# Kernel tuning notes

Hardware: AMD Instinct MI355X
Metric: run time of the kernel (lower is better)

The kernel has to match this reference:

```python
import jax, jax.numpy as jnp
import numpy as np

N_FLUID = 20000
N_BOX = 10000
PARTICLE_RADIUS = 0.025
FILTER_EXTENT = 1.5 * 6 * PARTICLE_RADIUS   # radius_scale * 6 * particle_radius = 0.225
RADIUS = 0.5 * FILTER_EXTENT                # neighbor search radius = 0.1125
DT = 1.0 / 50.0
KS = 4                                      # kernel size per axis
K3 = KS * KS * KS
LAYER_CH = [32, 64, 64, 3]
GRAVITY = jnp.array([0.0, -9.81, 0.0], jnp.float32)


def _radius_search(query, source, radius, exclude_self=False):
    """Brute-force (chunked) fixed radius search in numpy; returns (query_idx, src_idx)."""
    r2 = radius * radius
    s2 = (source ** 2).sum(1)
    qs, ss = [], []
    chunk = 2048
    for i0 in range(0, query.shape[0], chunk):
        q = query[i0:i0 + chunk]
        d2 = (q ** 2).sum(1)[:, None] + s2[None, :] - 2.0 * (q @ source.T)
        m = d2 < r2
        if exclude_self:  # radius_search_ignore_query_points=True
            rows = np.arange(q.shape[0])
            m[rows, i0 + rows] = False
        qq, sj = np.nonzero(m)
        qs.append((qq + i0).astype(np.int32))
        ss.append(sj.astype(np.int32))
    return np.concatenate(qs), np.concatenate(ss)


def _glorot(rng, shape):
    std = np.sqrt(2.0 / (shape[-2] + shape[-1]))
    return (rng.randn(*shape) * std).astype(np.float32)


def setup_inputs() -> dict:
    rng = np.random.RandomState(0)
    side = (N_FLUID / 8000.0) ** (1.0 / 3.0)  # rest density (2*particle_radius)^-3 = 8000/m^3
    pos = (rng.rand(N_FLUID, 3) * side).astype(np.float32)
    vel = (rng.randn(N_FLUID, 3) * 0.5).astype(np.float32)
    box = (rng.rand(N_BOX, 3) * side).astype(np.float32)
    bn = rng.randn(N_BOX, 3)
    box_feats = (bn / np.linalg.norm(bn, axis=1, keepdims=True)).astype(np.float32)
    # Neighbor search runs on gravity-integrated positions, exactly as in forward.
    g = np.array([0.0, -9.81, 0.0], np.float32)
    vel2 = vel + DT * g
    pos2 = pos + DT * (vel2 + vel) * 0.5
    ff_q, ff_s = _radius_search(pos2, pos2, RADIUS, exclude_self=True)
    fo_q, fo_s = _radius_search(pos2, box, RADIUS)
    inp = dict(pos=pos, vel=vel, box=box, box_feats=box_feats,
               ff_q=ff_q, ff_s=ff_s, fo_q=fo_q, fo_s=fo_s)
    inp['w_cf0'] = _glorot(rng, (KS, KS, KS, 4, LAYER_CH[0]))
    inp['w_co0'] = _glorot(rng, (KS, KS, KS, 3, LAYER_CH[0]))
    inp['w_d0'] = _glorot(rng, (4, LAYER_CH[0]))
    inp['b_d0'] = np.zeros(LAYER_CH[0], np.float32)
    in_chs = [3 * LAYER_CH[0], LAYER_CH[1], LAYER_CH[2]]
    for i in range(1, 4):
        ci, co = in_chs[i - 1], LAYER_CH[i]
        inp['w_c%d' % i] = _glorot(rng, (KS, KS, KS, ci, co))
        inp['w_d%d' % i] = _glorot(rng, (ci, co))
        inp['b_d%d' % i] = np.zeros(co, np.float32)
    return {k: jnp.asarray(v) for k, v in inp.items()}


def ball_to_cube(u):
    """Volume-preserving unit-ball -> unit-cube map (sphere->cylinder->cube). u: [E,3]."""
    x, y, z = u[:, 0], u[:, 1], u[:, 2]
    eps = 1e-12
    sq = x * x + y * y + z * z
    norm = jnp.sqrt(sq + eps)
    # sphere -> cylinder
    cap = 1.25 * z * z > x * x + y * y
    s_cap = jnp.sqrt(3.0 * norm / (norm + jnp.abs(z) + eps))
    s_side = norm / jnp.sqrt(x * x + y * y + eps)
    s = jnp.where(cap, s_cap, s_side)
    xc, yc = x * s, y * s
    zc = jnp.where(cap, jnp.sign(z) * norm, 1.5 * z)
    nz = sq > eps
    xc = jnp.where(nz, xc, 0.0)
    yc = jnp.where(nz, yc, 0.0)
    zc = jnp.where(nz, zc, 0.0)
    # cylinder -> cube: area-preserving (concentric) disc -> square on xy
    rxy = jnp.sqrt(xc * xc + yc * yc + eps)
    xbig = jnp.abs(yc) <= jnp.abs(xc)
    dx = jnp.where(jnp.abs(xc) > eps, xc, 1.0)
    dy = jnp.where(jnp.abs(yc) > eps, yc, 1.0)
    c4pi = 4.0 / jnp.pi
    tx = jnp.sign(xc) * rxy
    ty = jnp.sign(yc) * rxy
    xq = jnp.where(xbig, tx, ty * c4pi * jnp.arctan(xc / dy))
    yq = jnp.where(xbig, tx * c4pi * jnp.arctan(yc / dx), ty)
    nxy = xc * xc + yc * yc > eps
    xq = jnp.where(nxy, xq, 0.0)
    yq = jnp.where(nxy, yq, 0.0)
    return jnp.stack([xq, yq, zc], axis=-1)


def cconv(Wk, feat_src, q_idx, s_idx, pos_s, pos_q, nq):
    """ContinuousConv: window * trilinear kernel interp * gather, scatter-reduce to queries.
    Wk: [KS,KS,KS,Cin,Cout]. Returns [nq,Cout]."""
    d = (pos_s[s_idx] - pos_q[q_idx]) * (1.0 / RADIUS)    # [E,3] in unit ball
    r2 = jnp.sum(d * d, axis=-1)
    win = jnp.clip((1.0 - r2) ** 3, 0.0, 1.0)             # poly6 window
    g = (ball_to_cube(d) + 1.0) * (0.5 * (KS - 1))        # align_corners grid coords [0,KS-1]
    g0f = jnp.floor(g)
    f = g - g0f
    g0 = g0f.astype(jnp.int32)
    s = feat_src[s_idx] * win[:, None]                    # [E,Cin]
    cin = feat_src.shape[1]
    # accumulate per (query, kernel-cell) then one dense GEMM with the kernel
    G = jnp.zeros((nq * K3, cin), feat_src.dtype)
    for c in range(8):
        b = jnp.array([(c >> 2) & 1, (c >> 1) & 1, c & 1], jnp.int32)
        idx = jnp.clip(g0 + b[None, :], 0, KS - 1)        # [E,3]
        w = jnp.prod(jnp.where(b[None, :] == 1, f, 1.0 - f), axis=-1)  # trilinear wt [E]
        cell = (idx[:, 0] * KS + idx[:, 1]) * KS + idx[:, 2]
        G = G.at[q_idx * K3 + cell].add(w[:, None] * s)
    return jnp.einsum('nkc,kco->no', G.reshape(nq, K3, cin), Wk.reshape(K3, cin, -1))


def reference(pos, vel, box, box_feats, ff_q, ff_s, fo_q, fo_s,
              w_cf0, w_co0, w_d0, b_d0,
              w_c1, w_d1, b_d1, w_c2, w_d2, b_d2, w_c3, w_d3, b_d3):
    n = pos.shape[0]
    vel2 = vel + DT * GRAVITY
    pos2 = pos + DT * (vel2 + vel) * 0.5
    fl = jnp.concatenate([jnp.ones_like(pos[:, :1]), vel2], axis=-1)  # [N,4]
    a_cf = cconv(w_cf0, fl, ff_q, ff_s, pos2, pos2, n)
    a_co = cconv(w_co0, box_feats, fo_q, fo_s, box, pos2, n)
    a_df = fl @ w_d0 + b_d0
    x = jnp.concatenate([a_co, a_cf, a_df], axis=-1)  # [N,96]
    for wc, wd, bd in ((w_c1, w_d1, b_d1), (w_c2, w_d2, b_d2), (w_c3, w_d3, b_d3)):
        h = jax.nn.relu(x)
        y = cconv(wc, h, ff_q, ff_s, pos2, pos2, n) + h @ wd + bd
        x = y + x if y.shape[-1] == x.shape[-1] else y
    pos_correction = x * (1.0 / 128.0)
    pos_new = pos2 + pos_correction
    vel_new = (pos_new - pos) * (1.0 / DT)
    return pos_new, vel_new
```

## Files before the change

kernel.cpp:

```cpp
#include <hip/hip_runtime.h>
#include <algorithm>

#define DT_F 0.02f
#define INV_R (1.0f / 0.1125f)

typedef __attribute__((ext_vector_type(8))) short short8;
typedef __attribute__((ext_vector_type(4))) float float4v;

static inline int cdiv(int a, int b) { return (a + b - 1) / b; }

__device__ __forceinline__ float sgnf(float v) {
    return (v > 0.f) ? 1.f : ((v < 0.f) ? -1.f : 0.f);
}

__device__ __forceinline__ unsigned short f2bf(float f) {
    union { float f; unsigned u; } v; v.f = f;
    return (unsigned short)((v.u + 0x7fffu + ((v.u >> 16) & 1u)) >> 16);
}
__device__ __forceinline__ float bf2f(unsigned short h) {
    union { unsigned u; float f; } v; v.u = ((unsigned)h) << 16;
    return v.f;
}

__device__ __forceinline__ void ball_to_cube_dev(float x, float y, float z,
                                                 float& ox, float& oy, float& oz) {
    const float eps = 1e-12f;
    float sq = x * x + y * y + z * z;
    float nrm = sqrtf(sq + eps);
    float xy2 = x * x + y * y;
    bool cap = 1.25f * z * z > xy2;
    float s_cap = sqrtf(3.f * nrm / (nrm + fabsf(z) + eps));
    float s_side = nrm / sqrtf(xy2 + eps);
    float s = cap ? s_cap : s_side;
    float xc = x * s, yc = y * s;
    float zc = cap ? sgnf(z) * nrm : 1.5f * z;
    if (!(sq > eps)) { xc = 0.f; yc = 0.f; zc = 0.f; }
    float rxy = sqrtf(xc * xc + yc * yc + eps);
    bool xbig = fabsf(yc) <= fabsf(xc);
    float dx = (fabsf(xc) > eps) ? xc : 1.f;
    float dy = (fabsf(yc) > eps) ? yc : 1.f;
    const float c4pi = 1.27323954473516276f;
    float tx = sgnf(xc) * rxy, ty = sgnf(yc) * rxy;
    float xq = xbig ? tx : ty * c4pi * atanf(xc / dy);
    float yq = xbig ? tx * c4pi * atanf(yc / dx) : ty;
    if (!(xc * xc + yc * yc > eps)) { xq = 0.f; yq = 0.f; }
    ox = xq; oy = yq; oz = zc;
}

__global__ void prep_kernel(const float* __restrict__ pos, const float* __restrict__ vel,
                            int n, float* __restrict__ pos2, float* __restrict__ fl) {
    int i = blockIdx.x * blockDim.x + threadIdx.x;
    if (i >= n) return;
    float v0 = vel[i * 3 + 0], v1 = vel[i * 3 + 1], v2 = vel[i * 3 + 2];
    float u0 = v0, u1 = v1 + DT_F * (-9.81f), u2 = v2;
    pos2[i * 3 + 0] = pos[i * 3 + 0] + DT_F * (u0 + v0) * 0.5f;
    pos2[i * 3 + 1] = pos[i * 3 + 1] + DT_F * (u1 + v1) * 0.5f;
    pos2[i * 3 + 2] = pos[i * 3 + 2] + DT_F * (u2 + v2) * 0.5f;
    fl[i * 4 + 0] = 1.f;
    fl[i * 4 + 1] = u0;
    fl[i * 4 + 2] = u1;
    fl[i * 4 + 3] = u2;
}

__global__ void row_ptr_kernel(const int* __restrict__ q_idx, int E, int nq,
                               int* __restrict__ row_ptr) {
    int q = blockIdx.x * blockDim.x + threadIdx.x;
    if (q > nq) return;
    int lo = 0, hi = E;
    while (lo < hi) {
        int mid = (lo + hi) >> 1;
        if (q_idx[mid] < q) lo = mid + 1; else hi = mid;
    }
    row_ptr[q] = lo;
}

__global__ void edge_geom_kernel(const float* __restrict__ posq, const float* __restrict__ poss,
                                 const int* __restrict__ q_idx, const int* __restrict__ s_idx,
                                 int E, float* __restrict__ wgt, uint2* __restrict__ cells,
                                 uint4* __restrict__ edata) {
    int e = blockIdx.x * blockDim.x + threadIdx.x;
    if (e >= E) return;
    int q = q_idx[e], s = s_idx[e];
    float dx = (poss[s * 3 + 0] - posq[q * 3 + 0]) * INV_R;
    float dy = (poss[s * 3 + 1] - posq[q * 3 + 1]) * INV_R;
    float dz = (poss[s * 3 + 2] - posq[q * 3 + 2]) * INV_R;
    float r2 = dx * dx + dy * dy + dz * dz;
    float w1 = 1.f - r2;
    float win = fminf(fmaxf(w1 * w1 * w1, 0.f), 1.f);
    float bx, by, bz;
    ball_to_cube_dev(dx, dy, dz, bx, by, bz);
    float gx = (bx + 1.f) * 1.5f, gy = (by + 1.f) * 1.5f, gz = (bz + 1.f) * 1.5f;
    int ix = min(max((int)floorf(gx), 0), 2);
    int iy = min(max((int)floorf(gy), 0), 2);
    int iz = min(max((int)floorf(gz), 0), 2);
    float fx = gx - (float)ix, fy = gy - (float)iy, fz = gz - (float)iz;
    float wv[8];
    unsigned int cl[8];
#pragma unroll
    for (int c = 0; c < 8; c++) {
        int cbx = (c >> 2) & 1, cby = (c >> 1) & 1, cbz = c & 1;
        int jx = ix + cbx, jy = iy + cby, jz = iz + cbz;
        cl[c] = (unsigned int)((jx * 4 + jy) * 4 + jz);
        wv[c] = win * (cbx ? fx : 1.f - fx) * (cby ? fy : 1.f - fy) * (cbz ? fz : 1.f - fz);
    }
    float4* wp = (float4*)(wgt + (size_t)e * 8);
    wp[0] = make_float4(wv[0], wv[1], wv[2], wv[3]);
    wp[1] = make_float4(wv[4], wv[5], wv[6], wv[7]);
    uint2 cp;
    cp.x = cl[0] | (cl[1] << 8) | (cl[2] << 16) | (cl[3] << 24);
    cp.y = cl[4] | (cl[5] << 8) | (cl[6] << 16) | (cl[7] << 24);
    cells[e] = cp;
#pragma unroll
    for (int w = 0; w < 4; w++) {
        int pa = w >> 1, pb = w & 1;
        int cby = pa ^ (iy & 1), cbz = pb ^ (iz & 1);
        int cA = cby * 2 + cbz;
        uint4 d;
        d.x = __float_as_uint(wv[cA]);
        d.y = __float_as_uint(wv[cA + 4]);
        d.z = cl[cA] | (cl[cA + 4] << 8);
        d.w = (unsigned)s;
        edata[(size_t)w * E + e] = d;
    }
}

__global__ void dense0_kernel(const float* __restrict__ fl, const float* __restrict__ w,
                              const float* __restrict__ b, int n, float* __restrict__ x96) {
    int i = blockIdx.x * blockDim.x + threadIdx.x;
    if (i >= n * 32) return;
    int q = i >> 5, o = i & 31;
    float acc = b[o];
#pragma unroll
    for (int c = 0; c < 4; c++) acc += fl[q * 4 + c] * w[c * 32 + o];
    x96[(size_t)q * 96 + 64 + o] = acc;
}

__global__ void init_out_kernel(float* __restrict__ C, const float* __restrict__ bias,
                                const float* __restrict__ resid, int n, int co, int ldc) {
    int i = blockIdx.x * blockDim.x + threadIdx.x;
    if (i >= n * co) return;
    int q = i / co, o = i - q * co;
    float v = bias ? bias[o] : 0.f;
    if (resid) v += resid[(size_t)q * ldc + o];
    C[(size_t)q * ldc + o] = v;
}

__global__ void wt_kernel(const float* __restrict__ wc, const float* __restrict__ wd,
                          int ci, int co, int K, unsigned short* __restrict__ Wt) {
    int i = blockIdx.x * blockDim.x + threadIdx.x;
    if (i >= co * K) return;
    int n = i / K, k = i - n * K;
    float v = (k < 64 * ci) ? wc[(size_t)k * co + n] : wd[(size_t)(k - 64 * ci) * co + n];
    Wt[i] = f2bf(v);
}

__global__ void wt3_kernel(const float* __restrict__ wc, unsigned short* __restrict__ Wt) {
    int i = blockIdx.x * blockDim.x + threadIdx.x;
    if (i >= 192 * 64) return;
    int j = i >> 6, k = i & 63;
    int cell = j / 3, o = j - cell * 3;
    Wt[i] = f2bf(wc[((size_t)cell * 64 + k) * 3 + o]);
}

__global__ void relu_bf16_kernel(const float* __restrict__ x, int n,
                                 unsigned short* __restrict__ h) {
    int i = blockIdx.x * blockDim.x + threadIdx.x;
    if (i < n) h[i] = f2bf(fmaxf(x[i], 0.f));
}

template <int CIN>
__global__ __launch_bounds__(256) void build_G0_par(
    const float* __restrict__ feat, const uint4* __restrict__ edata, int E,
    const int* __restrict__ row_ptr, int q0, float* __restrict__ G) {
    __shared__ float Gs[4 * 64 * 8];
    int lq = blockIdx.x, q = q0 + lq, t = threadIdx.x;
    int wave = t >> 6, lane = t & 63;
    int j = lane >> 4, k = (lane >> 3) & 1, ch = lane & 7;
    for (int i = t; i < 2048; i += 256) Gs[i] = 0.f;
    __syncthreads();
    int e0 = row_ptr[q], e1 = row_ptr[q + 1];
    int cnt = e1 - e0;
    if (cnt > 0) {
        int last = e1 - 1;
        const uint4* ed = edata + (size_t)wave * E;
        int nIt = (cnt + 3) >> 2;
        uint4 dA = ed[min(e0 + j, last)];
        uint4 dB = ed[min(e0 + 4 + j, last)];
        float fA = (ch < CIN) ? feat[(size_t)dA.w * CIN + ch] : 0.f;
        float* Gr = Gs + j * 512;
        for (int i = 0; i < nIt; i++) {
            uint4 dC = ed[min(e0 + (i + 2) * 4 + j, last)];
            float fB = (ch < CIN) ? feat[(size_t)dB.w * CIN + ch] : 0.f;
            bool v = (e0 + i * 4 + j) < e1;
            float w = v ? (k ? __uint_as_float(dA.y) : __uint_as_float(dA.x)) : 0.f;
            int cell = (int)((dA.z >> (k * 8)) & 255u);
            Gr[cell * 8 + ch] += w * fA;
            dA = dB; dB = dC; fA = fB;
        }
    }
    __syncthreads();
    size_t base = (size_t)lq * 64 * CIN;
    for (int i = t; i < 64 * CIN; i += 256) {
        int cell = i / CIN, c = i - cell * CIN;
        int o = cell * 8 + c;
        G[base + i] = Gs[o] + Gs[512 + o] + Gs[1024 + o] + Gs[1536 + o];
    }
}

template <int CIN>
__global__ __launch_bounds__(256) void build_G_mfma(
    const unsigned short* __restrict__ hb,
    const float* __restrict__ wgt, const uint2* __restrict__ cells,
    const int* __restrict__ s_idx, const int* __restrict__ row_ptr,
    int q0, unsigned short* __restrict__ G) {
    constexpr int LDK = 72;
    constexpr int CP = CIN / 2;
    constexpr int NT = CIN / 16;
    __shared__ unsigned short S[64 * LDK];
    __shared__ unsigned short Ft[CIN * LDK];
    int lq = blockIdx.x, q = q0 + lq, t = threadIdx.x;
    int wave = t >> 6, lane = t & 63;
    int e0 = row_ptr[q], e1 = row_ptr[q + 1];
    int nE = e1 - e0;
    float4v acc[NT];
#pragma unroll
    for (int i = 0; i < NT; i++) acc[i] = (float4v){0.f, 0.f, 0.f, 0.f};

    for (int c0 = 0; c0 < nE; c0 += 64) {
        int cnt = min(64, nE - c0);
        __syncthreads();
        for (int i = t; i < 64 * LDK / 2; i += 256) ((unsigned int*)S)[i] = 0u;
        for (int i = t; i < 64 * CP; i += 256) {
            int e = i / CP, cp = i - e * CP;
            unsigned v = 0u;
            if (e < cnt) {
                int s = s_idx[e0 + c0 + e];
                v = ((const unsigned int*)hb)[(size_t)s * CP + cp];
            }
            Ft[(2 * cp) * LDK + e] = (unsigned short)(v & 0xffffu);
            Ft[(2 * cp + 1) * LDK + e] = (unsigned short)(v >> 16);
        }
        {
            int e = t >> 2, cpair = t & 3;
            if (e < cnt) {
                int ee = e0 + c0 + e;
                uint2 cp = cells[ee];
                float w0 = wgt[(size_t)ee * 8 + cpair * 2];
                float w1 = wgt[(size_t)ee * 8 + cpair * 2 + 1];
                unsigned word = (cpair < 2) ? cp.x : cp.y;
                int sh = (cpair & 1) * 16;
                int cell0 = (int)((word >> sh) & 255u);
                int cell1 = (int)((word >> (sh + 8)) & 255u);
                S[cell0 * LDK + e] = f2bf(w0);
                S[cell1 * LDK + e] = f2bf(w1);
            }
        }
        __syncthreads();
        int kq = lane >> 4, mrow = lane & 15;
#pragma unroll
        for (int ks = 0; ks < 2; ks++) {
            int kk = ks * 32 + kq * 8;
            short8 a = *(const short8*)(S + (wave * 16 + mrow) * LDK + kk);
#pragma unroll
            for (int nt = 0; nt < NT; nt++) {
                short8 b = *(const short8*)(Ft + (nt * 16 + mrow) * LDK + kk);
                acc[nt] = __builtin_amdgcn_mfma_f32_16x16x32_bf16(a, b, acc[nt], 0, 0, 0);
            }
        }
    }
    unsigned short* Go = G + (size_t)lq * (size_t)(65 * CIN);
    int col = lane & 15, rq = lane >> 4;
#pragma unroll
    for (int nt = 0; nt < NT; nt++) {
#pragma unroll
        for (int r = 0; r < 4; r++) {
            int cell = wave * 16 + rq * 4 + r;
            Go[cell * CIN + nt * 16 + col] = f2bf(acc[nt][r]);
        }
    }
    if (t < CP) {
        ((unsigned int*)(Go + 64 * CIN))[t] = ((const unsigned int*)hb)[(size_t)q * CP + t];
    }
}

__global__ __launch_bounds__(256) void gemm_mfma(
    const unsigned short* __restrict__ A, const unsigned short* __restrict__ Wt,
    float* __restrict__ C, int M, int K, int ldc, int kpb) {
    int wave = threadIdx.x >> 6, lane = threadIdx.x & 63;
    int m0 = blockIdx.x * 64;
    int kbeg = blockIdx.y * kpb;
    int kend = min(K, kbeg + kpb);
    int mrow = lane & 15, kq = lane >> 4;
    int n0 = wave * 16;
    const unsigned short* Bp = Wt + (size_t)(n0 + mrow) * K;
    float4v acc[4] = {{0.f, 0.f, 0.f, 0.f}, {0.f, 0.f, 0.f, 0.f},
                      {0.f, 0.f, 0.f, 0.f}, {0.f, 0.f, 0.f, 0.f}};
    int r0 = min(m0 + mrow, M - 1);
    int r1 = min(m0 + 16 + mrow, M - 1);
    int r2 = min(m0 + 32 + mrow, M - 1);
    int r3 = min(m0 + 48 + mrow, M - 1);
    const unsigned short* A0 = A + (size_t)r0 * K;
    const unsigned short* A1 = A + (size_t)r1 * K;
    const unsigned short* A2 = A + (size_t)r2 * K;
    const unsigned short* A3 = A + (size_t)r3 * K;
    for (int k0 = kbeg; k0 < kend; k0 += 32) {
        int kk = k0 + kq * 8;
        short8 b = *(const short8*)(Bp + kk);
        short8 a0 = *(const short8*)(A0 + kk);
        short8 a1 = *(const short8*)(A1 + kk);
        short8 a2 = *(const short8*)(A2 + kk);
        short8 a3 = *(const short8*)(A3 + kk);
        acc[0] = __builtin_amdgcn_mfma_f32_16x16x32_bf16(a0, b, acc[0], 0, 0, 0);
        acc[1] = __builtin_amdgcn_mfma_f32_16x16x32_bf16(a1, b, acc[1], 0, 0, 0);
        acc[2] = __builtin_amdgcn_mfma_f32_16x16x32_bf16(a2, b, acc[2], 0, 0, 0);
        acc[3] = __builtin_amdgcn_mfma_f32_16x16x32_bf16(a3, b, acc[3], 0, 0, 0);
    }
    int col = lane & 15, rq = lane >> 4;
#pragma unroll
    for (int mt = 0; mt < 4; mt++) {
#pragma unroll
        for (int r = 0; r < 4; r++) {
            int m = m0 + mt * 16 + rq * 4 + r;
            if (m < M) atomicAdd(&C[(size_t)m * ldc + n0 + col], acc[mt][r]);
        }
    }
}

__global__ __launch_bounds__(256) void gemm_mfma_store(
    const unsigned short* __restrict__ A, const unsigned short* __restrict__ Wt,
    float* __restrict__ C, int M, int K, int ldc) {
    int wave = threadIdx.x >> 6, lane = threadIdx.x & 63;
    int m0 = blockIdx.x * 64;
    int n0 = blockIdx.y * 64 + wave * 16;
    int mrow = lane & 15, kq = lane >> 4;
    const unsigned short* Bp = Wt + (size_t)(n0 + mrow) * K;
    float4v acc[4] = {{0.f, 0.f, 0.f, 0.f}, {0.f, 0.f, 0.f, 0.f},
                      {0.f, 0.f, 0.f, 0.f}, {0.f, 0.f, 0.f, 0.f}};
    int r0 = min(m0 + mrow, M - 1);
    int r1 = min(m0 + 16 + mrow, M - 1);
    int r2 = min(m0 + 32 + mrow, M - 1);
    int r3 = min(m0 + 48 + mrow, M - 1);
    const unsigned short* A0 = A + (size_t)r0 * K;
    const unsigned short* A1 = A + (size_t)r1 * K;
    const unsigned short* A2 = A + (size_t)r2 * K;
    const unsigned short* A3 = A + (size_t)r3 * K;
    for (int k0 = 0; k0 < K; k0 += 32) {
        int kk = k0 + kq * 8;
        short8 b = *(const short8*)(Bp + kk);
        short8 a0 = *(const short8*)(A0 + kk);
        short8 a1 = *(const short8*)(A1 + kk);
        short8 a2 = *(const short8*)(A2 + kk);
        short8 a3 = *(const short8*)(A3 + kk);
        acc[0] = __builtin_amdgcn_mfma_f32_16x16x32_bf16(a0, b, acc[0], 0, 0, 0);
        acc[1] = __builtin_amdgcn_mfma_f32_16x16x32_bf16(a1, b, acc[1], 0, 0, 0);
        acc[2] = __builtin_amdgcn_mfma_f32_16x16x32_bf16(a2, b, acc[2], 0, 0, 0);
        acc[3] = __builtin_amdgcn_mfma_f32_16x16x32_bf16(a3, b, acc[3], 0, 0, 0);
    }
    int col = lane & 15, rq = lane >> 4;
#pragma unroll
    for (int mt = 0; mt < 4; mt++) {
#pragma unroll
        for (int r = 0; r < 4; r++) {
            int m = m0 + mt * 16 + rq * 4 + r;
            if (m < M) C[(size_t)m * ldc + n0 + col] = acc[mt][r];
        }
    }
}

__global__ __launch_bounds__(256) void conv3_reduce(
    const float* __restrict__ P,
    const float* __restrict__ wgt, const uint2* __restrict__ cells,
    const int* __restrict__ s_idx, const int* __restrict__ row_ptr,
    const unsigned short* __restrict__ hq, const float* __restrict__ wd3,
    const float* __restrict__ b3, int n, float* __restrict__ y3) {
    int wave = threadIdx.x >> 6, lane = threadIdx.x & 63;
    int q = blockIdx.x * 4 + wave;
    if (q >= n) return;
    float a0 = 0.f, a1 = 0.f, a2 = 0.f;
    int e0 = row_ptr[q], e1 = row_ptr[q + 1];
    for (int e = e0 + lane; e < e1; e += 64) {
        int s = s_idx[e];
        uint2 cp = cells[e];
        const float4* wp = (const float4*)(wgt + (size_t)e * 8);
        float4 wa = wp[0], wb = wp[1];
        const float* Ps = P + (size_t)s * 192;
        float wv[8] = {wa.x, wa.y, wa.z, wa.w, wb.x, wb.y, wb.z, wb.w};
#pragma unroll
        for (int c = 0; c < 8; c++) {
            unsigned word = (c < 4) ? cp.x : cp.y;
            int cell = (int)((word >> ((c & 3) * 8)) & 255u);
            const float* pc = Ps + cell * 3;
            a0 += wv[c] * pc[0];
            a1 += wv[c] * pc[1];
            a2 += wv[c] * pc[2];
        }
    }
    float hv = bf2f(hq[(size_t)q * 64 + lane]);
    a0 += hv * wd3[lane * 3 + 0];
    a1 += hv * wd3[lane * 3 + 1];
    a2 += hv * wd3[lane * 3 + 2];
#pragma unroll
    for (int off = 32; off > 0; off >>= 1) {
        a0 += __shfl_xor(a0, off);
        a1 += __shfl_xor(a1, off);
        a2 += __shfl_xor(a2, off);
    }
    if (lane == 0) {
        y3[(size_t)q * 3 + 0] = a0 + b3[0];
        y3[(size_t)q * 3 + 1] = a1 + b3[1];
        y3[(size_t)q * 3 + 2] = a2 + b3[2];
    }
}

template <int BM, int BN, int BK, int TM, int TN>
__global__ void gemm_atomic(const float* __restrict__ A, const float* __restrict__ B,
                            float* __restrict__ C, int M, int N, int K,
                            int ldc, int coff, int kpb) {
    constexpr int THREADS = (BM / TM) * (BN / TN);
    __shared__ float As[BK][BM + 1];
    __shared__ float Bs[BK][BN + 1];
    int tx = threadIdx.x;
    int tcols = BN / TN;
    int tcol = tx % tcols, trow = tx / tcols;
    int m0 = blockIdx.x * BM;
    int kbeg = blockIdx.y * kpb;
    int kend = min(K, kbeg + kpb);
    float acc[TM][TN];
#pragma unroll
    for (int i = 0; i < TM; i++)
#pragma unroll
        for (int j = 0; j < TN; j++) acc[i][j] = 0.f;
    for (int k0 = kbeg; k0 < kend; k0 += BK) {
        for (int i = tx; i < BM * BK; i += THREADS) {
            int kk = i % BK, mm = i / BK;
            int m = m0 + mm, k = k0 + kk;
            As[kk][mm] = (m < M && k < K) ? A[(size_t)m * K + k] : 0.f;
        }
        for (int i = tx; i < BN * BK; i += THREADS) {
            int nn = i % BN, kk = i / BN;
            int k = k0 + kk;
            Bs[kk][nn] = (k < K && nn < N) ? B[(size_t)k * N + nn] : 0.f;
        }
        __syncthreads();
#pragma unroll
        for (int kk = 0; kk < BK; kk++) {
            float a[TM], b[TN];
#pragma unroll
            for (int i = 0; i < TM; i++) a[i] = As[kk][trow * TM + i];
#pragma unroll
            for (int j = 0; j < TN; j++) b[j] = Bs[kk][tcol * TN + j];
#pragma unroll
            for (int i = 0; i < TM; i++)
#pragma unroll
                for (int j = 0; j < TN; j++) acc[i][j] += a[i] * b[j];
        }
        __syncthreads();
    }
    for (int i = 0; i < TM; i++) {
        int m = m0 + trow * TM + i;
        if (m >= M) continue;
        for (int j = 0; j < TN; j++) {
            int nn = tcol * TN + j;
            if (nn >= N) continue;
            atomicAdd(&C[(size_t)m * ldc + coff + nn], acc[i][j]);
        }
    }
}

__global__ void final_kernel(const float* __restrict__ pos, const float* __restrict__ pos2,
                             const float* __restrict__ y3, int n, float* __restrict__ out) {
    int i = blockIdx.x * blockDim.x + threadIdx.x;
    if (i >= n * 3) return;
    float pn = pos2[i] + y3[i] * (1.f / 128.f);
    out[i] = pn;
    out[n * 3 + i] = (pn - pos[i]) * (1.f / DT_F);
}

extern "C" void kernel_launch(void* const* d_in, const int* in_sizes, int n_in,
                              void* d_out, int out_size, void* d_ws, size_t ws_size,
                              hipStream_t stream) {
    const float* pos       = (const float*)d_in[0];
    const float* vel       = (const float*)d_in[1];
    const float* box       = (const float*)d_in[2];
    const float* box_feats = (const float*)d_in[3];
    const int*   ff_q      = (const int*)d_in[4];
    const int*   ff_s      = (const int*)d_in[5];
    const int*   fo_q      = (const int*)d_in[6];
    const int*   fo_s      = (const int*)d_in[7];
    const float* w_cf0     = (const float*)d_in[8];
    const float* w_co0     = (const float*)d_in[9];
    const float* w_d0      = (const float*)d_in[10];
    const float* b_d0      = (const float*)d_in[11];
    const float* w_c1      = (const float*)d_in[12];
    const float* w_d1      = (const float*)d_in[13];
    const float* b_d1      = (const float*)d_in[14];
    const float* w_c2      = (const float*)d_in[15];
    const float* w_d2      = (const float*)d_in[16];
    const float* b_d2      = (const float*)d_in[17];
    const float* w_c3      = (const float*)d_in[18];
    const float* w_d3      = (const float*)d_in[19];
    const float* b_d3      = (const float*)d_in[20];
    float* out = (float*)d_out;

    int n   = in_sizes[0] / 3;
    int Eff = in_sizes[4];
    int Efo = in_sizes[6];

    float* base = (float*)d_ws;
    size_t off = 0;
    auto alloc = [&](size_t nf) { float* p = base + off; off += (nf + 3) & ~(size_t)3; return p; };
    float* pos2  = alloc((size_t)n * 3);
    float* fl    = alloc((size_t)n * 4);
    float* x96   = alloc((size_t)n * 96);
    float* x64a  = alloc((size_t)n * 64);
    float* x64b  = alloc((size_t)n * 64);
    float* y3    = alloc((size_t)n * 3);
    int* rp_ff   = (int*)alloc((size_t)n + 1);
    int* rp_fo   = (int*)alloc((size_t)n + 1);
    unsigned short* Wt   = (unsigned short*)alloc((size_t)65 * 96 * 64 / 2);
    unsigned short* Wt3  = (unsigned short*)alloc((size_t)192 * 64 / 2);
    unsigned short* hb96 = (unsigned short*)alloc((size_t)n * 48);
    unsigned short* hb64 = (unsigned short*)alloc((size_t)n * 32);
    float* P3    = alloc((size_t)n * 192);
    float* wgt_ff = alloc((size_t)Eff * 8);
    uint2* cl_ff  = (uint2*)alloc((size_t)Eff * 2);
    float* wgt_fo = alloc((size_t)Efo * 8);
    uint2* cl_fo  = (uint2*)alloc((size_t)Efo * 2);
    uint4* ed_ff  = (uint4*)alloc((size_t)Eff * 16);
    uint4* ed_fo  = (uint4*)alloc((size_t)Efo * 16);
    float* G = base + off;
    unsigned short* Gb = (unsigned short*)G;

    size_t totalF = ws_size / sizeof(float);
    size_t availF = (totalF > off) ? (totalF - off) : 0;
    auto chunkQ = [&](size_t floatsPerQ) {
        long q = (long)(availF / floatsPerQ);
        if (q < 1) q = 1;
        if (q > n) q = n;
        return (int)q;
    };

    prep_kernel<<<cdiv(n, 256), 256, 0, stream>>>(pos, vel, n, pos2, fl);
    row_ptr_kernel<<<cdiv(n + 1, 256), 256, 0, stream>>>(ff_q, Eff, n, rp_ff);
    row_ptr_kernel<<<cdiv(n + 1, 256), 256, 0, stream>>>(fo_q, Efo, n, rp_fo);
    edge_geom_kernel<<<cdiv(Eff, 256), 256, 0, stream>>>(pos2, pos2, ff_q, ff_s, Eff, wgt_ff, cl_ff, ed_ff);
    edge_geom_kernel<<<cdiv(Efo, 256), 256, 0, stream>>>(pos2, box, fo_q, fo_s, Efo, wgt_fo, cl_fo, ed_fo);

    init_out_kernel<<<cdiv(n * 64, 256), 256, 0, stream>>>(x96, nullptr, nullptr, n, 64, 96);
    dense0_kernel<<<cdiv(n * 32, 256), 256, 0, stream>>>(fl, w_d0, b_d0, n, x96);
    {
        int Q = chunkQ(64 * 4);
        for (int q0 = 0; q0 < n; q0 += Q) {
            int mc = std::min(Q, n - q0);
            build_G0_par<4><<<mc, 256, 0, stream>>>(fl, ed_ff, Eff, rp_ff, q0, G);
            gemm_atomic<64, 32, 16, 4, 2><<<dim3(cdiv(mc, 64), 2), 256, 0, stream>>>(
                G, w_cf0, x96 + (size_t)q0 * 96, mc, 32, 256, 96, 32, 8 * 16);
        }
    }
    {
        int Q = chunkQ(64 * 3);
        for (int q0 = 0; q0 < n; q0 += Q) {
            int mc = std::min(Q, n - q0);
            build_G0_par<3><<<mc, 256, 0, stream>>>(box_feats, ed_fo, Efo, rp_fo, q0, G);
            gemm_atomic<64, 32, 16, 4, 2><<<dim3(cdiv(mc, 64), 2), 256, 0, stream>>>(
                G, w_co0, x96 + (size_t)q0 * 96, mc, 32, 192, 96, 0, 6 * 16);
        }
    }

    {
        const int K = 65 * 96;
        wt_kernel<<<cdiv(64 * K, 256), 256, 0, stream>>>(w_c1, w_d1, 96, 64, K, Wt);
        init_out_kernel<<<cdiv(n * 64, 256), 256, 0, stream>>>(x64a, b_d1, nullptr, n, 64, 64);
        relu_bf16_kernel<<<cdiv(n * 96, 256), 256, 0, stream>>>(x96, n * 96, hb96);
        int Q = chunkQ((size_t)K / 2);
        for (int q0 = 0; q0 < n; q0 += Q) {
            int mc = std::min(Q, n - q0);
            build_G_mfma<96><<<mc, 256, 0, stream>>>(
                hb96, wgt_ff, cl_ff, ff_s, rp_ff, q0, Gb);
            gemm_mfma<<<dim3(cdiv(mc, 64), 4), 256, 0, stream>>>(
                Gb, Wt, x64a + (size_t)q0 * 64, mc, K, 64, cdiv(K / 32, 4) * 32);
        }
    }

    {
        const int K = 65 * 64;
        wt_kernel<<<cdiv(64 * K, 256), 256, 0, stream>>>(w_c2, w_d2, 64, 64, K, Wt);
        init_out_kernel<<<cdiv(n * 64, 256), 256, 0, stream>>>(x64b, b_d2, x64a, n, 64, 64);
        relu_bf16_kernel<<<cdiv(n * 64, 256), 256, 0, stream>>>(x64a, n * 64, hb64);
        int Q = chunkQ((size_t)K / 2);
        for (int q0 = 0; q0 < n; q0 += Q) {
            int mc = std::min(Q, n - q0);
            build_G_mfma<64><<<mc, 256, 0, stream>>>(
                hb64, wgt_ff, cl_ff, ff_s, rp_ff, q0, Gb);
            gemm_mfma<<<dim3(cdiv(mc, 64), 4), 256, 0, stream>>>(
                Gb, Wt, x64b + (size_t)q0 * 64, mc, K, 64, cdiv(K / 32, 4) * 32);
        }
    }

    {
        relu_bf16_kernel<<<cdiv(n * 64, 256), 256, 0, stream>>>(x64b, n * 64, hb64);
        wt3_kernel<<<cdiv(192 * 64, 256), 256, 0, stream>>>(w_c3, Wt3);
        gemm_mfma_store<<<dim3(cdiv(n, 64), 3), 256, 0, stream>>>(hb64, Wt3, P3, n, 64, 192);
        conv3_reduce<<<cdiv(n, 4), 256, 0, stream>>>(
            P3, wgt_ff, cl_ff, ff_s, rp_ff, hb64, w_d3, b_d3, n, y3);
    }

    final_kernel<<<cdiv(n * 3, 256), 256, 0, stream>>>(pos, pos2, y3, n, out);
}
```

Baseline: 877.8 us.

## Route first-layer continuous convolutions through bf16 MFMA gather and GEMM path

Replaces the fp32 scalar build_G0_par plus atomic fp32 GEMM for the first fluid and box convolutions with the existing bf16 MFMA build_G/gemm_mfma path. Input features are padded to 16 channels in bf16, and the dense0 layer is folded into the fluid GEMM as an extra weight slot. The per-edge edata scatter buffer is no longer written by edge_geom. This removes the scalar FMA work, the atomics and the extra edge-data traffic. In exchange it adds padding waste (16 lanes for 3-4 real channels) and bf16 rounding in the first layer.

```diff
diff --git a/kernel.cpp b/kernel.cpp
--- a/kernel.cpp
+++ b/kernel.cpp
@@ -76,8 +76,7 @@
 
 __global__ void edge_geom_kernel(const float* __restrict__ posq, const float* __restrict__ poss,
                                  const int* __restrict__ q_idx, const int* __restrict__ s_idx,
-                                 int E, float* __restrict__ wgt, uint2* __restrict__ cells,
-                                 uint4* __restrict__ edata) {
+                                 int E, float* __restrict__ wgt, uint2* __restrict__ cells) {
     int e = blockIdx.x * blockDim.x + threadIdx.x;
     if (e >= E) return;
     int q = q_idx[e], s = s_idx[e];
@@ -110,29 +109,13 @@
     cp.x = cl[0] | (cl[1] << 8) | (cl[2] << 16) | (cl[3] << 24);
     cp.y = cl[4] | (cl[5] << 8) | (cl[6] << 16) | (cl[7] << 24);
     cells[e] = cp;
-#pragma unroll
-    for (int w = 0; w < 4; w++) {
-        int pa = w >> 1, pb = w & 1;
-        int cby = pa ^ (iy & 1), cbz = pb ^ (iz & 1);
-        int cA = cby * 2 + cbz;
-        uint4 d;
-        d.x = __float_as_uint(wv[cA]);
-        d.y = __float_as_uint(wv[cA + 4]);
-        d.z = cl[cA] | (cl[cA + 4] << 8);
-        d.w = (unsigned)s;
-        edata[(size_t)w * E + e] = d;
-    }
-}
-
-__global__ void dense0_kernel(const float* __restrict__ fl, const float* __restrict__ w,
-                              const float* __restrict__ b, int n, float* __restrict__ x96) {
-    int i = blockIdx.x * blockDim.x + threadIdx.x;
-    if (i >= n * 32) return;
-    int q = i >> 5, o = i & 31;
-    float acc = b[o];
-#pragma unroll
-    for (int c = 0; c < 4; c++) acc += fl[q * 4 + c] * w[c * 32 + o];
-    x96[(size_t)q * 96 + 64 + o] = acc;
+}
+
+__global__ void init_x96_kernel(float* __restrict__ x96, const float* __restrict__ b0, int n) {
+    int i = blockIdx.x * blockDim.x + threadIdx.x;
+    if (i >= n * 96) return;
+    int o = i % 96;
+    x96[i] = (o >= 64) ? b0[o - 64] : 0.f;
 }
 
 __global__ void init_out_kernel(float* __restrict__ C, const float* __restrict__ bias,
@@ -154,6 +137,31 @@
     Wt[i] = f2bf(v);
 }
 
+__global__ void wt0f_kernel(const float* __restrict__ wcf, const float* __restrict__ wd,
+                            unsigned short* __restrict__ Wt) {
+    int i = blockIdx.x * blockDim.x + threadIdx.x;
+    if (i >= 64 * 1056) return;
+    int nrow = i / 1056, k = i - nrow * 1056;
+    int slot = k >> 4, c = k & 15;
+    float v = 0.f;
+    if (nrow < 32) {
+        if (slot < 64 && c < 4) v = wcf[((size_t)slot * 4 + c) * 32 + nrow];
+    } else {
+        if (slot == 64 && c < 4) v = wd[c * 32 + (nrow - 32)];
+    }
+    Wt[i] = f2bf(v);
+}
+
+__global__ void wt0b_kernel(const float* __restrict__ wco, unsigned short* __restrict__ Wt) {
+    int i = blockIdx.x * blockDim.x + threadIdx.x;
+    if (i >= 64 * 1056) return;
+    int nrow = i / 1056, k = i - nrow * 1056;
+    int slot = k >> 4, c = k & 15;
+    float v = 0.f;
+    if (nrow < 32 && slot < 64 && c < 3) v = wco[((size_t)slot * 3 + c) * 32 + nrow];
+    Wt[i] = f2bf(v);
+}
+
 __global__ void wt3_kernel(const float* __restrict__ wc, unsigned short* __restrict__ Wt) {
     int i = blockIdx.x * blockDim.x + threadIdx.x;
     if (i >= 192 * 64) return;
@@ -168,46 +176,15 @@
     if (i < n) h[i] = f2bf(fmaxf(x[i], 0.f));
 }
 
-template <int CIN>
-__global__ __launch_bounds__(256) void build_G0_par(
-    const float* __restrict__ feat, const uint4* __restrict__ edata, int E,
-    const int* __restrict__ row_ptr, int q0, float* __restrict__ G) {
-    __shared__ float Gs[4 * 64 * 8];
-    int lq = blockIdx.x, q = q0 + lq, t = threadIdx.x;
-    int wave = t >> 6, lane = t & 63;
-    int j = lane >> 4, k = (lane >> 3) & 1, ch = lane & 7;
-    for (int i = t; i < 2048; i += 256) Gs[i] = 0.f;
-    __syncthreads();
-    int e0 = row_ptr[q], e1 = row_ptr[q + 1];
-    int cnt = e1 - e0;
-    if (cnt > 0) {
-        int last = e1 - 1;
-        const uint4* ed = edata + (size_t)wave * E;
-        int nIt = (cnt + 3) >> 2;
-        uint4 dA = ed[min(e0 + j, last)];
-        uint4 dB = ed[min(e0 + 4 + j, last)];
-        float fA = (ch < CIN) ? feat[(size_t)dA.w * CIN + ch] : 0.f;
-        float* Gr = Gs + j * 512;
-        for (int i = 0; i < nIt; i++) {
-            uint4 dC = ed[min(e0 + (i + 2) * 4 + j, last)];
-            float fB = (ch < CIN) ? feat[(size_t)dB.w * CIN + ch] : 0.f;
-            bool v = (e0 + i * 4 + j) < e1;
-            float w = v ? (k ? __uint_as_float(dA.y) : __uint_as_float(dA.x)) : 0.f;
-            int cell = (int)((dA.z >> (k * 8)) & 255u);
-            Gr[cell * 8 + ch] += w * fA;
-            dA = dB; dB = dC; fA = fB;
-        }
-    }
-    __syncthreads();
-    size_t base = (size_t)lq * 64 * CIN;
-    for (int i = t; i < 64 * CIN; i += 256) {
-        int cell = i / CIN, c = i - cell * CIN;
-        int o = cell * 8 + c;
-        G[base + i] = Gs[o] + Gs[512 + o] + Gs[1024 + o] + Gs[1536 + o];
-    }
-}
-
-template <int CIN>
+__global__ void pad16_bf16(const float* __restrict__ src, int n, int c,
+                           unsigned short* __restrict__ dst) {
+    int i = blockIdx.x * blockDim.x + threadIdx.x;
+    if (i >= n * 16) return;
+    int q = i >> 4, k = i & 15;
+    dst[i] = (k < c) ? f2bf(src[q * c + k]) : (unsigned short)0;
+}
+
+template <int CIN, int SLOTS>
 __global__ __launch_bounds__(256) void build_G_mfma(
     const unsigned short* __restrict__ hb,
     const float* __restrict__ wgt, const uint2* __restrict__ cells,
@@ -268,7 +245,7 @@
             }
         }
     }
-    unsigned short* Go = G + (size_t)lq * (size_t)(65 * CIN);
+    unsigned short* Go = G + (size_t)lq * (size_t)(SLOTS * CIN);
     int col = lane & 15, rq = lane >> 4;
 #pragma unroll
     for (int nt = 0; nt < NT; nt++) {
@@ -280,6 +257,9 @@
     }
     if (t < CP) {
         ((unsigned int*)(Go + 64 * CIN))[t] = ((const unsigned int*)hb)[(size_t)q * CP + t];
+    }
+    if (SLOTS > 65) {
+        if (t < (SLOTS - 65) * CP) ((unsigned int*)(Go + 65 * CIN))[t] = 0u;
     }
 }
 
@@ -412,61 +392,6 @@
     }
 }
 
-template <int BM, int BN, int BK, int TM, int TN>
-__global__ void gemm_atomic(const float* __restrict__ A, const float* __restrict__ B,
-                            float* __restrict__ C, int M, int N, int K,
-                            int ldc, int coff, int kpb) {
-    constexpr int THREADS = (BM / TM) * (BN / TN);
-    __shared__ float As[BK][BM + 1];
-    __shared__ float Bs[BK][BN + 1];
-    int tx = threadIdx.x;
-    int tcols = BN / TN;
-    int tcol = tx % tcols, trow = tx / tcols;
-    int m0 = blockIdx.x * BM;
-    int kbeg = blockIdx.y * kpb;
-    int kend = min(K, kbeg + kpb);
-    float acc[TM][TN];
-#pragma unroll
-    for (int i = 0; i < TM; i++)
-#pragma unroll
-        for (int j = 0; j < TN; j++) acc[i][j] = 0.f;
-    for (int k0 = kbeg; k0 < kend; k0 += BK) {
-        for (int i = tx; i < BM * BK; i += THREADS) {
-            int kk = i % BK, mm = i / BK;
-            int m = m0 + mm, k = k0 + kk;
-            As[kk][mm] = (m < M && k < K) ? A[(size_t)m * K + k] : 0.f;
-        }
-        for (int i = tx; i < BN * BK; i += THREADS) {
-            int nn = i % BN, kk = i / BN;
-            int k = k0 + kk;
-            Bs[kk][nn] = (k < K && nn < N) ? B[(size_t)k * N + nn] : 0.f;
-        }
-        __syncthreads();
-#pragma unroll
-        for (int kk = 0; kk < BK; kk++) {
-            float a[TM], b[TN];
-#pragma unroll
-            for (int i = 0; i < TM; i++) a[i] = As[kk][trow * TM + i];
-#pragma unroll
-            for (int j = 0; j < TN; j++) b[j] = Bs[kk][tcol * TN + j];
-#pragma unroll
-            for (int i = 0; i < TM; i++)
-#pragma unroll
-                for (int j = 0; j < TN; j++) acc[i][j] += a[i] * b[j];
-        }
-        __syncthreads();
-    }
-    for (int i = 0; i < TM; i++) {
-        int m = m0 + trow * TM + i;
-        if (m >= M) continue;
-        for (int j = 0; j < TN; j++) {
-            int nn = tcol * TN + j;
-            if (nn >= N) continue;
-            atomicAdd(&C[(size_t)m * ldc + coff + nn], acc[i][j]);
-        }
-    }
-}
-
 __global__ void final_kernel(const float* __restrict__ pos, const float* __restrict__ pos2,
                              const float* __restrict__ y3, int n, float* __restrict__ out) {
     int i = blockIdx.x * blockDim.x + threadIdx.x;
@@ -503,6 +428,7 @@
     float* out = (float*)d_out;
 
     int n   = in_sizes[0] / 3;
+    int nb  = in_sizes[2] / 3;
     int Eff = in_sizes[4];
     int Efo = in_sizes[6];
 
@@ -519,6 +445,8 @@
     int* rp_fo   = (int*)alloc((size_t)n + 1);
     unsigned short* Wt   = (unsigned short*)alloc((size_t)65 * 96 * 64 / 2);
     unsigned short* Wt3  = (unsigned short*)alloc((size_t)192 * 64 / 2);
+    unsigned short* flb  = (unsigned short*)alloc((size_t)n * 8);
+    unsigned short* bxb  = (unsigned short*)alloc((size_t)nb * 8);
     unsigned short* hb96 = (unsigned short*)alloc((size_t)n * 48);
     unsigned short* hb64 = (unsigned short*)alloc((size_t)n * 32);
     float* P3    = alloc((size_t)n * 192);
@@ -526,10 +454,7 @@
     uint2* cl_ff  = (uint2*)alloc((size_t)Eff * 2);
     float* wgt_fo = alloc((size_t)Efo * 8);
     uint2* cl_fo  = (uint2*)alloc((size_t)Efo * 2);
-    uint4* ed_ff  = (uint4*)alloc((size_t)Eff * 16);
-    uint4* ed_fo  = (uint4*)alloc((size_t)Efo * 16);
-    float* G = base + off;
-    unsigned short* Gb = (unsigned short*)G;
+    unsigned short* Gb = (unsigned short*)(base + off);
 
     size_t totalF = ws_size / sizeof(float);
     size_t availF = (totalF > off) ? (totalF - off) : 0;
@@ -543,27 +468,30 @@
     prep_kernel<<<cdiv(n, 256), 256, 0, stream>>>(pos, vel, n, pos2, fl);
     row_ptr_kernel<<<cdiv(n + 1, 256), 256, 0, stream>>>(ff_q, Eff, n, rp_ff);
     row_ptr_kernel<<<cdiv(n + 1, 256), 256, 0, stream>>>(fo_q, Efo, n, rp_fo);
-    edge_geom_kernel<<<cdiv(Eff, 256), 256, 0, stream>>>(pos2, pos2, ff_q, ff_s, Eff, wgt_ff, cl_ff, ed_ff);
-    edge_geom_kernel<<<cdiv(Efo, 256), 256, 0, stream>>>(pos2, box, fo_q, fo_s, Efo, wgt_fo, cl_fo, ed_fo);
-
-    init_out_kernel<<<cdiv(n * 64, 256), 256, 0, stream>>>(x96, nullptr, nullptr, n, 64, 96);
-    dense0_kernel<<<cdiv(n * 32, 256), 256, 0, stream>>>(fl, w_d0, b_d0, n, x96);
+    edge_geom_kernel<<<cdiv(Eff, 256), 256, 0, stream>>>(pos2, pos2, ff_q, ff_s, Eff, wgt_ff, cl_ff);
+    edge_geom_kernel<<<cdiv(Efo, 256), 256, 0, stream>>>(pos2, box, fo_q, fo_s, Efo, wgt_fo, cl_fo);
+
+    init_x96_kernel<<<cdiv(n * 96, 256), 256, 0, stream>>>(x96, b_d0, n);
+    pad16_bf16<<<cdiv(n * 16, 256), 256, 0, stream>>>(fl, n, 4, flb);
+    pad16_bf16<<<cdiv(nb * 16, 256), 256, 0, stream>>>(box_feats, nb, 3, bxb);
     {
-        int Q = chunkQ(64 * 4);
+        const int K = 66 * 16;
+        int Q = chunkQ((size_t)K / 2);
+        wt0f_kernel<<<cdiv(64 * K, 256), 256, 0, stream>>>(w_cf0, w_d0, Wt);
         for (int q0 = 0; q0 < n; q0 += Q) {
             int mc = std::min(Q, n - q0);
-            build_G0_par<4><<<mc, 256, 0, stream>>>(fl, ed_ff, Eff, rp_ff, q0, G);
-            gemm_atomic<64, 32, 16, 4, 2><<<dim3(cdiv(mc, 64), 2), 256, 0, stream>>>(
-                G, w_cf0, x96 + (size_t)q0 * 96, mc, 32, 256, 96, 32, 8 * 16);
-        }
-    }
-    {
-        int Q = chunkQ(64 * 3);
+            build_G_mfma<16, 66><<<mc, 256, 0, stream>>>(
+                flb, wgt_ff, cl_ff, ff_s, rp_ff, q0, Gb);
+            gemm_mfma<<<dim3(cdiv(mc, 64), 4), 256, 0, stream>>>(
+                Gb, Wt, x96 + (size_t)q0 * 96 + 32, mc, K, 96, cdiv(K / 32, 4) * 32);
+        }
+        wt0b_kernel<<<cdiv(64 * K, 256), 256, 0, stream>>>(w_co0, Wt);
         for (int q0 = 0; q0 < n; q0 += Q) {
             int mc = std::min(Q, n - q0);
-            build_G0_par<3><<<mc, 256, 0, stream>>>(box_feats, ed_fo, Efo, rp_fo, q0, G);
-            gemm_atomic<64, 32, 16, 4, 2><<<dim3(cdiv(mc, 64), 2), 256, 0, stream>>>(
-                G, w_co0, x96 + (size_t)q0 * 96, mc, 32, 192, 96, 0, 6 * 16);
+            build_G_mfma<16, 66><<<mc, 256, 0, stream>>>(
+                bxb, wgt_fo, cl_fo, fo_s, rp_fo, q0, Gb);
+            gemm_mfma<<<dim3(cdiv(mc, 64), 4), 256, 0, stream>>>(
+                Gb, Wt, x96 + (size_t)q0 * 96, mc, K, 96, cdiv(K / 32, 4) * 32);
         }
     }
 
@@ -575,7 +503,7 @@
         int Q = chunkQ((size_t)K / 2);
         for (int q0 = 0; q0 < n; q0 += Q) {
             int mc = std::min(Q, n - q0);
-            build_G_mfma<96><<<mc, 256, 0, stream>>>(
+            build_G_mfma<96, 65><<<mc, 256, 0, stream>>>(
                 hb96, wgt_ff, cl_ff, ff_s, rp_ff, q0, Gb);
             gemm_mfma<<<dim3(cdiv(mc, 64), 4), 256, 0, stream>>>(
                 Gb, Wt, x64a + (size_t)q0 * 64, mc, K, 64, cdiv(K / 32, 4) * 32);
@@ -590,7 +518,7 @@
         int Q = chunkQ((size_t)K / 2);
         for (int q0 = 0; q0 < n; q0 += Q) {
             int mc = std::min(Q, n - q0);
-            build_G_mfma<64><<<mc, 256, 0, stream>>>(
+            build_G_mfma<64, 65><<<mc, 256, 0, stream>>>(
                 hb64, wgt_ff, cl_ff, ff_s, rp_ff, q0, Gb);
             gemm_mfma<<<dim3(cdiv(mc, 64), 4), 256, 0, stream>>>(
                 Gb, Wt, x64b + (size_t)q0 * 64, mc, K, 64, cdiv(K / 32, 4) * 32);
```

New measurement: 828.6 us. -5.6%, faster.
